# Kernel optimization log

Hardware: AMD Instinct MI355X
Metric: run time of the kernel (lower is better)

Reference implementation:

```python
import jax, jax.numpy as jnp
import numpy as np

D_IN = 256
DIMS = 256


def setup_inputs() -> dict:
    key = jax.random.key(0)
    k1, k2, k3, k4, k5 = jax.random.split(key, 5)
    B, Tq, Tk = 4, 512, 512
    query = jax.random.normal(k1, (B, Tq, D_IN), dtype=jnp.float32)
    value = jax.random.normal(k2, (B, Tk, D_IN), dtype=jnp.float32)
    # Dense(dims, use_bias=False) kernels (glorot-like scale) and AdditiveAttention scale vector
    Wq = jax.random.normal(k3, (D_IN, DIMS), dtype=jnp.float32) / np.sqrt(D_IN)
    Wv = jax.random.normal(k4, (D_IN, DIMS), dtype=jnp.float32) / np.sqrt(D_IN)
    scale = jax.random.normal(k5, (DIMS,), dtype=jnp.float32)
    return {"query": query, "value": value, "Wq": Wq, "Wv": Wv, "scale": scale}


def reference(query, value, Wq, Wv, scale):
    # q_proj: [B,Tq,d], k_proj: [B,Tk,d]; attention value = RAW value tensor (as in source)
    q = jnp.einsum("bqi,id->bqd", query, Wq)
    k = jnp.einsum("bki,id->bkd", value, Wv)
    # Additive (Bahdanau) scores: [B,Tq,Tk] via broadcast tanh then reduce with scale
    scores = jnp.einsum("bqkd,d->bqk", jnp.tanh(q[:, :, None, :] + k[:, None, :, :]), scale)
    attn = jax.nn.softmax(scores, axis=-1)  # masks are all-ones -> no-op
    out = jnp.einsum("bqk,bki->bqi", attn, value)
    return out, attn
```

## Files before the change

### kernel.cpp

```cpp
#include <hip/hip_runtime.h>

#define LOG2E 1.4426950408889634f
#define TWO_LOG2E 2.885390081777927f

__device__ __forceinline__ float fast_exp2(float x) { return __builtin_amdgcn_exp2f(x); }
__device__ __forceinline__ float fast_rcp(float x)  { return __builtin_amdgcn_rcpf(x); }

__device__ __forceinline__ void term2(float s0, float s1, float qx, float qy,
                                      float kx, float ky, float& acc) {
    const float A = fmaf(qx, kx, 1.f);
    const float B = fmaf(qy, ky, 1.f);
    acc = fmaf(fmaf(s1, A, s0 * B), fast_rcp(A * B), acc);
}

__global__ __launch_bounds__(256) void proj_kernel(
    const float* __restrict__ query, const float* __restrict__ value,
    const float* __restrict__ Wq, const float* __restrict__ Wv,
    float* __restrict__ eq, float* __restrict__ ekT)
{
    __shared__ float in_lds[8 * 256];
    const int t = threadIdx.x;
    const int row0 = blockIdx.x * 8;
    const float* src; const float* W;
    if (row0 < 2048) { src = query + (size_t)row0 * 256; W = Wq; }
    else { src = value + (size_t)(row0 - 2048) * 256; W = Wv; }

    const float4* s4 = (const float4*)src;
    float4* l4 = (float4*)in_lds;
    l4[t] = s4[t];
    l4[t + 256] = s4[t + 256];
    __syncthreads();

    float acc[8];
#pragma unroll
    for (int r = 0; r < 8; ++r) acc[r] = 0.f;

    for (int d = 0; d < 256; d += 4) {
        const float w0 = W[(d + 0) * 256 + t];
        const float w1 = W[(d + 1) * 256 + t];
        const float w2 = W[(d + 2) * 256 + t];
        const float w3 = W[(d + 3) * 256 + t];
#pragma unroll
        for (int r = 0; r < 8; ++r) {
            const float4 v = *(const float4*)&in_lds[r * 256 + d];
            acc[r] = fmaf(v.x, w0, acc[r]);
            acc[r] = fmaf(v.y, w1, acc[r]);
            acc[r] = fmaf(v.z, w2, acc[r]);
            acc[r] = fmaf(v.w, w3, acc[r]);
        }
    }

    if (row0 < 2048) {
        float* dst = eq + (size_t)row0 * 256;
#pragma unroll
        for (int r = 0; r < 8; ++r) dst[r * 256 + t] = fast_exp2(acc[r] * TWO_LOG2E);
    } else {
        const int r0 = row0 - 2048;
        const int bb = r0 >> 9, kin = r0 & 511;
        float* dstT = ekT + (size_t)bb * 131072 + (size_t)t * 512 + kin;
        float4 v0, v1;
        v0.x = fast_exp2(acc[0] * TWO_LOG2E); v0.y = fast_exp2(acc[1] * TWO_LOG2E);
        v0.z = fast_exp2(acc[2] * TWO_LOG2E); v0.w = fast_exp2(acc[3] * TWO_LOG2E);
        v1.x = fast_exp2(acc[4] * TWO_LOG2E); v1.y = fast_exp2(acc[5] * TWO_LOG2E);
        v1.z = fast_exp2(acc[6] * TWO_LOG2E); v1.w = fast_exp2(acc[7] * TWO_LOG2E);
        *(float4*)dstT = v0;
        *(float4*)(dstT + 4) = v1;
    }
}

#define EQ_ST 260
#define SS_ST 520
__global__ __launch_bounds__(512, 4) void fused_kernel(
    const float* __restrict__ eq, const float* __restrict__ ekT,
    const float* __restrict__ scale, const float* __restrict__ value,
    float* __restrict__ attn, float* __restrict__ out)
{
    __shared__ float eq_lds[4 * EQ_ST];
    __shared__ float sc_lds[256];
    __shared__ float s_tile[4 * SS_ST];
    __shared__ float red[4 * 4 * 256];
    __shared__ float inv_lds[4];

    const int t = threadIdx.x;
    const int w = t >> 6, lane = t & 63;
    const int qg = w >> 2;
    const int kg = ((w & 3) << 6) + lane;
    const int k0 = 2 * kg;
    const int qt = blockIdx.x, b = blockIdx.y;
    const int q0 = qt * 4;

    if (t < 256) {
        const int row = t >> 6, c = t & 63;
        const float4 v = ((const float4*)(eq + (size_t)(b * 512 + q0) * 256))[t];
        *(float4*)&eq_lds[row * EQ_ST + 4 * c] = v;
    } else {
        sc_lds[t - 256] = -2.f * scale[t - 256];
    }
    __syncthreads();

    const float* ekTb = ekT + (size_t)b * 131072;
    const float* q0r = &eq_lds[(2 * qg + 0) * EQ_ST];
    const float* q1r = &eq_lds[(2 * qg + 1) * EQ_ST];

    float a00 = 0.f, a01 = 0.f, a10 = 0.f, a11 = 0.f;

    float4 sv  = *(const float4*)&sc_lds[0];
    float4 qv0 = *(const float4*)&q0r[0];
    float4 qv1 = *(const float4*)&q1r[0];
    float2 k0v = *(const float2*)&ekTb[(size_t)0 * 512 + k0];
    float2 k1v = *(const float2*)&ekTb[(size_t)1 * 512 + k0];
    float2 k2v = *(const float2*)&ekTb[(size_t)2 * 512 + k0];
    float2 k3v = *(const float2*)&ekTb[(size_t)3 * 512 + k0];

#pragma unroll 4
    for (int d = 0; d < 256; d += 4) {
        const float4 csv = sv, c0 = qv0, c1 = qv1;
        const float2 ck0 = k0v, ck1 = k1v, ck2 = k2v, ck3 = k3v;

        if (d < 252) {
            const int dn = d + 4;
            sv  = *(const float4*)&sc_lds[dn];
            qv0 = *(const float4*)&q0r[dn];
            qv1 = *(const float4*)&q1r[dn];
            k0v = *(const float2*)&ekTb[(size_t)(dn + 0) * 512 + k0];
            k1v = *(const float2*)&ekTb[(size_t)(dn + 1) * 512 + k0];
            k2v = *(const float2*)&ekTb[(size_t)(dn + 2) * 512 + k0];
            k3v = *(const float2*)&ekTb[(size_t)(dn + 3) * 512 + k0];
        }

        term2(csv.x, csv.y, c0.x, c0.y, ck0.x, ck1.x, a00);
        term2(csv.z, csv.w, c0.z, c0.w, ck2.x, ck3.x, a00);
        term2(csv.x, csv.y, c0.x, c0.y, ck0.y, ck1.y, a01);
        term2(csv.z, csv.w, c0.z, c0.w, ck2.y, ck3.y, a01);

        term2(csv.x, csv.y, c1.x, c1.y, ck0.x, ck1.x, a10);
        term2(csv.z, csv.w, c1.z, c1.w, ck2.x, ck3.x, a10);
        term2(csv.x, csv.y, c1.x, c1.y, ck0.y, ck1.y, a11);
        term2(csv.z, csv.w, c1.z, c1.w, ck2.y, ck3.y, a11);
    }

    *(float2*)&s_tile[(2 * qg + 0) * SS_ST + k0] = make_float2(a00, a01);
    *(float2*)&s_tile[(2 * qg + 1) * SS_ST + k0] = make_float2(a10, a11);
    __syncthreads();

    if (w < 4) {
        float x[8];
        float m = -1e30f;
#pragma unroll
        for (int j = 0; j < 8; ++j) {
            x[j] = s_tile[w * SS_ST + 64 * j + lane];
            m = fmaxf(m, x[j]);
        }
#pragma unroll
        for (int off = 32; off; off >>= 1) m = fmaxf(m, __shfl_xor(m, off));

        float sum = 0.f;
#pragma unroll
        for (int j = 0; j < 8; ++j) { x[j] = fast_exp2((x[j] - m) * LOG2E); sum += x[j]; }
#pragma unroll
        for (int off = 32; off; off >>= 1) sum += __shfl_xor(sum, off);
        const float inv = fast_rcp(sum);

        float* arow = attn + (size_t)(b * 512 + q0 + w) * 512;
#pragma unroll
        for (int j = 0; j < 8; ++j) {
            s_tile[w * SS_ST + 64 * j + lane] = x[j];
            arow[64 * j + lane] = x[j] * inv;
        }
        if (lane == 0) inv_lds[w] = inv;
    }
    __syncthreads();

    float4 acc[4];
#pragma unroll
    for (int r = 0; r < 4; ++r) acc[r] = make_float4(0.f, 0.f, 0.f, 0.f);

    const float* vbase = value + (size_t)(b * 512 + 64 * w) * 256;
    for (int k4 = 0; k4 < 64; k4 += 4) {
        const float4 v0 = *(const float4*)&vbase[(k4 + 0) * 256 + lane * 4];
        const float4 v1 = *(const float4*)&vbase[(k4 + 1) * 256 + lane * 4];
        const float4 v2 = *(const float4*)&vbase[(k4 + 2) * 256 + lane * 4];
        const float4 v3 = *(const float4*)&vbase[(k4 + 3) * 256 + lane * 4];
#pragma unroll
        for (int r = 0; r < 4; ++r) {
            const float4 s4 = *(const float4*)&s_tile[r * SS_ST + 64 * w + k4];
            acc[r].x = fmaf(s4.x, v0.x, acc[r].x); acc[r].y = fmaf(s4.x, v0.y, acc[r].y);
            acc[r].z = fmaf(s4.x, v0.z, acc[r].z); acc[r].w = fmaf(s4.x, v0.w, acc[r].w);
            acc[r].x = fmaf(s4.y, v1.x, acc[r].x); acc[r].y = fmaf(s4.y, v1.y, acc[r].y);
            acc[r].z = fmaf(s4.y, v1.z, acc[r].z); acc[r].w = fmaf(s4.y, v1.w, acc[r].w);
            acc[r].x = fmaf(s4.z, v2.x, acc[r].x); acc[r].y = fmaf(s4.z, v2.y, acc[r].y);
            acc[r].z = fmaf(s4.z, v2.z, acc[r].z); acc[r].w = fmaf(s4.z, v2.w, acc[r].w);
            acc[r].x = fmaf(s4.w, v3.x, acc[r].x); acc[r].y = fmaf(s4.w, v3.y, acc[r].y);
            acc[r].z = fmaf(s4.w, v3.z, acc[r].z); acc[r].w = fmaf(s4.w, v3.w, acc[r].w);
        }
    }

    if (w >= 4) {
#pragma unroll
        for (int r = 0; r < 4; ++r)
            *(float4*)&red[((w - 4) * 4 + r) * 256 + lane * 4] = acc[r];
    }
    __syncthreads();
    if (w < 4) {
#pragma unroll
        for (int r = 0; r < 4; ++r) {
            const float4 o = *(const float4*)&red[(w * 4 + r) * 256 + lane * 4];
            acc[r].x += o.x; acc[r].y += o.y; acc[r].z += o.z; acc[r].w += o.w;
        }
    }
    __syncthreads();
    if (w >= 2 && w < 4) {
#pragma unroll
        for (int r = 0; r < 4; ++r)
            *(float4*)&red[((w - 2) * 4 + r) * 256 + lane * 4] = acc[r];
    }
    __syncthreads();
    if (w < 2) {
#pragma unroll
        for (int r = 0; r < 4; ++r) {
            const float4 o = *(const float4*)&red[(w * 4 + r) * 256 + lane * 4];
            acc[r].x += o.x; acc[r].y += o.y; acc[r].z += o.z; acc[r].w += o.w;
        }
    }
    __syncthreads();
    if (w == 1) {
#pragma unroll
        for (int r = 0; r < 4; ++r)
            *(float4*)&red[r * 256 + lane * 4] = acc[r];
    }
    __syncthreads();
    if (w == 0) {
#pragma unroll
        for (int r = 0; r < 4; ++r) {
            const float4 o = *(const float4*)&red[r * 256 + lane * 4];
            const float iv = inv_lds[r];
            float4 res;
            res.x = (acc[r].x + o.x) * iv;
            res.y = (acc[r].y + o.y) * iv;
            res.z = (acc[r].z + o.z) * iv;
            res.w = (acc[r].w + o.w) * iv;
            *(float4*)&out[(size_t)(b * 512 + q0 + r) * 256 + lane * 4] = res;
        }
    }
}

extern "C" void kernel_launch(void* const* d_in, const int* in_sizes, int n_in,
                              void* d_out, int out_size, void* d_ws, size_t ws_size,
                              hipStream_t stream) {
    const float* query = (const float*)d_in[0];
    const float* value = (const float*)d_in[1];
    const float* Wq    = (const float*)d_in[2];
    const float* Wv    = (const float*)d_in[3];
    const float* scale = (const float*)d_in[4];

    float* out0 = (float*)d_out;
    float* attn = out0 + 4 * 512 * 256;

    float* eq  = (float*)d_ws;
    float* ekT = eq + 2048 * 256;

    proj_kernel<<<512, 256, 0, stream>>>(query, value, Wq, Wv, eq, ekT);
    fused_kernel<<<dim3(128, 4), 512, 0, stream>>>(eq, ekT, scale, value, attn, out0);
}
```

Measured before the change: 74.25 us.

## Tile value projection with coalesced transposed stores and halve fused block size

The value-projection half of proj_kernel now uses a 64x32 LDS-tiled GEMM and stages its output through LDS, so the transposed ekT writes are coalesced float4 rows instead of strided per-thread writes. The fused kernel drops from 512 to 256 threads per block, with each thread computing all four query rows against its two keys. This reuses each ekT load across four queries rather than two and removes one level of the cross-wave output reduction. The cost is more registers per thread and fewer waves per block for hiding latency.

```diff
diff --git a/kernel.cpp b/kernel.cpp
--- a/kernel.cpp
+++ b/kernel.cpp
@@ -19,58 +19,110 @@
     float* __restrict__ eq, float* __restrict__ ekT)
 {
     __shared__ float in_lds[8 * 256];
+    __shared__ float v_lds[64 * 68];
+    __shared__ float w_lds[64 * 36];
+    __shared__ float t_lds[32 * 68];
+
     const int t = threadIdx.x;
-    const int row0 = blockIdx.x * 8;
-    const float* src; const float* W;
-    if (row0 < 2048) { src = query + (size_t)row0 * 256; W = Wq; }
-    else { src = value + (size_t)(row0 - 2048) * 256; W = Wv; }
-
-    const float4* s4 = (const float4*)src;
-    float4* l4 = (float4*)in_lds;
-    l4[t] = s4[t];
-    l4[t + 256] = s4[t + 256];
-    __syncthreads();
-
-    float acc[8];
-#pragma unroll
-    for (int r = 0; r < 8; ++r) acc[r] = 0.f;
-
-    for (int d = 0; d < 256; d += 4) {
-        const float w0 = W[(d + 0) * 256 + t];
-        const float w1 = W[(d + 1) * 256 + t];
-        const float w2 = W[(d + 2) * 256 + t];
-        const float w3 = W[(d + 3) * 256 + t];
-#pragma unroll
-        for (int r = 0; r < 8; ++r) {
-            const float4 v = *(const float4*)&in_lds[r * 256 + d];
-            acc[r] = fmaf(v.x, w0, acc[r]);
-            acc[r] = fmaf(v.y, w1, acc[r]);
-            acc[r] = fmaf(v.z, w2, acc[r]);
-            acc[r] = fmaf(v.w, w3, acc[r]);
-        }
-    }
-
-    if (row0 < 2048) {
+    const int bx = blockIdx.x;
+
+    if (bx < 256) {
+        const int row0 = bx * 8;
+        const float4* s4 = (const float4*)(query + (size_t)row0 * 256);
+        float4* l4 = (float4*)in_lds;
+        l4[t] = s4[t];
+        l4[t + 256] = s4[t + 256];
+        __syncthreads();
+
+        float acc[8];
+#pragma unroll
+        for (int r = 0; r < 8; ++r) acc[r] = 0.f;
+
+        for (int d = 0; d < 256; d += 4) {
+            const float w0 = Wq[(d + 0) * 256 + t];
+            const float w1 = Wq[(d + 1) * 256 + t];
+            const float w2 = Wq[(d + 2) * 256 + t];
+            const float w3 = Wq[(d + 3) * 256 + t];
+#pragma unroll
+            for (int r = 0; r < 8; ++r) {
+                const float4 v = *(const float4*)&in_lds[r * 256 + d];
+                acc[r] = fmaf(v.x, w0, acc[r]);
+                acc[r] = fmaf(v.y, w1, acc[r]);
+                acc[r] = fmaf(v.z, w2, acc[r]);
+                acc[r] = fmaf(v.w, w3, acc[r]);
+            }
+        }
         float* dst = eq + (size_t)row0 * 256;
 #pragma unroll
         for (int r = 0; r < 8; ++r) dst[r * 256 + t] = fast_exp2(acc[r] * TWO_LOG2E);
     } else {
-        const int r0 = row0 - 2048;
-        const int bb = r0 >> 9, kin = r0 & 511;
-        float* dstT = ekT + (size_t)bb * 131072 + (size_t)t * 512 + kin;
-        float4 v0, v1;
-        v0.x = fast_exp2(acc[0] * TWO_LOG2E); v0.y = fast_exp2(acc[1] * TWO_LOG2E);
-        v0.z = fast_exp2(acc[2] * TWO_LOG2E); v0.w = fast_exp2(acc[3] * TWO_LOG2E);
-        v1.x = fast_exp2(acc[4] * TWO_LOG2E); v1.y = fast_exp2(acc[5] * TWO_LOG2E);
-        v1.z = fast_exp2(acc[6] * TWO_LOG2E); v1.w = fast_exp2(acc[7] * TWO_LOG2E);
-        *(float4*)dstT = v0;
-        *(float4*)(dstT + 4) = v1;
+        const int bi = bx - 256;
+        const int kt = bi >> 3, dt = bi & 7;
+        const int gk0 = kt * 64;
+        const int bb = gk0 >> 9, kin0 = gk0 & 511;
+        const int dout0 = dt * 32;
+        const int kp = t >> 3, dg = t & 7;
+
+        float acc[2][4];
+#pragma unroll
+        for (int i = 0; i < 2; ++i)
+#pragma unroll
+            for (int j = 0; j < 4; ++j) acc[i][j] = 0.f;
+
+        for (int dc = 0; dc < 256; dc += 64) {
+            __syncthreads();
+#pragma unroll
+            for (int l = 0; l < 4; ++l) {
+                const int idx = t + 256 * l;
+                const int r = idx >> 4, c4 = (idx & 15) * 4;
+                *(float4*)&v_lds[r * 68 + c4] =
+                    *(const float4*)&value[(size_t)(gk0 + r) * 256 + dc + c4];
+            }
+#pragma unroll
+            for (int l = 0; l < 2; ++l) {
+                const int idx = t + 256 * l;
+                const int r = idx >> 3, c4 = (idx & 7) * 4;
+                *(float4*)&w_lds[r * 36 + c4] =
+                    *(const float4*)&Wv[(size_t)(dc + r) * 256 + dout0 + c4];
+            }
+            __syncthreads();
+
+#pragma unroll 8
+            for (int din = 0; din < 64; ++din) {
+                const float v0 = v_lds[(2 * kp + 0) * 68 + din];
+                const float v1 = v_lds[(2 * kp + 1) * 68 + din];
+                const float4 wv = *(const float4*)&w_lds[din * 36 + 4 * dg];
+                acc[0][0] = fmaf(v0, wv.x, acc[0][0]);
+                acc[0][1] = fmaf(v0, wv.y, acc[0][1]);
+                acc[0][2] = fmaf(v0, wv.z, acc[0][2]);
+                acc[0][3] = fmaf(v0, wv.w, acc[0][3]);
+                acc[1][0] = fmaf(v1, wv.x, acc[1][0]);
+                acc[1][1] = fmaf(v1, wv.y, acc[1][1]);
+                acc[1][2] = fmaf(v1, wv.z, acc[1][2]);
+                acc[1][3] = fmaf(v1, wv.w, acc[1][3]);
+            }
+        }
+        __syncthreads();
+#pragma unroll
+        for (int i = 0; i < 2; ++i)
+#pragma unroll
+            for (int j = 0; j < 4; ++j)
+                t_lds[(4 * dg + j) * 68 + 2 * kp + i] =
+                    fast_exp2(acc[i][j] * TWO_LOG2E);
+        __syncthreads();
+#pragma unroll
+        for (int l = 0; l < 2; ++l) {
+            const int idx = t + 256 * l;
+            const int row = idx >> 4, c4 = (idx & 15) * 4;
+            *(float4*)&ekT[(size_t)bb * 131072 + (size_t)(dout0 + row) * 512 + kin0 + c4] =
+                *(const float4*)&t_lds[row * 68 + c4];
+        }
     }
 }
 
 #define EQ_ST 260
 #define SS_ST 520
-__global__ __launch_bounds__(512, 4) void fused_kernel(
+__global__ __launch_bounds__(256, 3) void fused_kernel(
     const float* __restrict__ eq, const float* __restrict__ ekT,
     const float* __restrict__ scale, const float* __restrict__ value,
     float* __restrict__ attn, float* __restrict__ out)
@@ -78,43 +130,46 @@
     __shared__ float eq_lds[4 * EQ_ST];
     __shared__ float sc_lds[256];
     __shared__ float s_tile[4 * SS_ST];
-    __shared__ float red[4 * 4 * 256];
+    __shared__ float red[2 * 4 * 256];
     __shared__ float inv_lds[4];
 
     const int t = threadIdx.x;
     const int w = t >> 6, lane = t & 63;
-    const int qg = w >> 2;
-    const int kg = ((w & 3) << 6) + lane;
+    const int kg = (w << 6) + lane;
     const int k0 = 2 * kg;
     const int qt = blockIdx.x, b = blockIdx.y;
     const int q0 = qt * 4;
 
-    if (t < 256) {
+    {
+        const float4 v = ((const float4*)(eq + (size_t)(b * 512 + q0) * 256))[t];
         const int row = t >> 6, c = t & 63;
-        const float4 v = ((const float4*)(eq + (size_t)(b * 512 + q0) * 256))[t];
         *(float4*)&eq_lds[row * EQ_ST + 4 * c] = v;
-    } else {
-        sc_lds[t - 256] = -2.f * scale[t - 256];
-    }
-    __syncthreads();
-
-    const float* ekTb = ekT + (size_t)b * 131072;
-    const float* q0r = &eq_lds[(2 * qg + 0) * EQ_ST];
-    const float* q1r = &eq_lds[(2 * qg + 1) * EQ_ST];
+    }
+    sc_lds[t] = -2.f * scale[t];
+    __syncthreads();
+
+    const float* ekTb = ekT + (size_t)b * 131072 + k0;
+    const float* q0r = &eq_lds[0 * EQ_ST];
+    const float* q1r = &eq_lds[1 * EQ_ST];
+    const float* q2r = &eq_lds[2 * EQ_ST];
+    const float* q3r = &eq_lds[3 * EQ_ST];
 
     float a00 = 0.f, a01 = 0.f, a10 = 0.f, a11 = 0.f;
+    float a20 = 0.f, a21 = 0.f, a30 = 0.f, a31 = 0.f;
 
     float4 sv  = *(const float4*)&sc_lds[0];
     float4 qv0 = *(const float4*)&q0r[0];
     float4 qv1 = *(const float4*)&q1r[0];
-    float2 k0v = *(const float2*)&ekTb[(size_t)0 * 512 + k0];
-    float2 k1v = *(const float2*)&ekTb[(size_t)1 * 512 + k0];
-    float2 k2v = *(const float2*)&ekTb[(size_t)2 * 512 + k0];
-    float2 k3v = *(const float2*)&ekTb[(size_t)3 * 512 + k0];
+    float4 qv2 = *(const float4*)&q2r[0];
+    float4 qv3 = *(const float4*)&q3r[0];
+    float2 k0v = *(const float2*)&ekTb[(size_t)0 * 512];
+    float2 k1v = *(const float2*)&ekTb[(size_t)1 * 512];
+    float2 k2v = *(const float2*)&ekTb[(size_t)2 * 512];
+    float2 k3v = *(const float2*)&ekTb[(size_t)3 * 512];
 
 #pragma unroll 4
     for (int d = 0; d < 256; d += 4) {
-        const float4 csv = sv, c0 = qv0, c1 = qv1;
+        const float4 csv = sv, c0 = qv0, c1 = qv1, c2 = qv2, c3 = qv3;
         const float2 ck0 = k0v, ck1 = k1v, ck2 = k2v, ck3 = k3v;
 
         if (d < 252) {
@@ -122,10 +177,12 @@
             sv  = *(const float4*)&sc_lds[dn];
             qv0 = *(const float4*)&q0r[dn];
             qv1 = *(const float4*)&q1r[dn];
-            k0v = *(const float2*)&ekTb[(size_t)(dn + 0) * 512 + k0];
-            k1v = *(const float2*)&ekTb[(size_t)(dn + 1) * 512 + k0];
-            k2v = *(const float2*)&ekTb[(size_t)(dn + 2) * 512 + k0];
-            k3v = *(const float2*)&ekTb[(size_t)(dn + 3) * 512 + k0];
+            qv2 = *(const float4*)&q2r[dn];
+            qv3 = *(const float4*)&q3r[dn];
+            k0v = *(const float2*)&ekTb[(size_t)(dn + 0) * 512];
+            k1v = *(const float2*)&ekTb[(size_t)(dn + 1) * 512];
+            k2v = *(const float2*)&ekTb[(size_t)(dn + 2) * 512];
+            k3v = *(const float2*)&ekTb[(size_t)(dn + 3) * 512];
         }
 
         term2(csv.x, csv.y, c0.x, c0.y, ck0.x, ck1.x, a00);
@@ -137,13 +194,25 @@
         term2(csv.z, csv.w, c1.z, c1.w, ck2.x, ck3.x, a10);
         term2(csv.x, csv.y, c1.x, c1.y, ck0.y, ck1.y, a11);
         term2(csv.z, csv.w, c1.z, c1.w, ck2.y, ck3.y, a11);
-    }
-
-    *(float2*)&s_tile[(2 * qg + 0) * SS_ST + k0] = make_float2(a00, a01);
-    *(float2*)&s_tile[(2 * qg + 1) * SS_ST + k0] = make_float2(a10, a11);
-    __syncthreads();
-
-    if (w < 4) {
+
+        term2(csv.x, csv.y, c2.x, c2.y, ck0.x, ck1.x, a20);
+        term2(csv.z, csv.w, c2.z, c2.w, ck2.x, ck3.x, a20);
+        term2(csv.x, csv.y, c2.x, c2.y, ck0.y, ck1.y, a21);
+        term2(csv.z, csv.w, c2.z, c2.w, ck2.y, ck3.y, a21);
+
+        term2(csv.x, csv.y, c3.x, c3.y, ck0.x, ck1.x, a30);
+        term2(csv.z, csv.w, c3.z, c3.w, ck2.x, ck3.x, a30);
+        term2(csv.x, csv.y, c3.x, c3.y, ck0.y, ck1.y, a31);
+        term2(csv.z, csv.w, c3.z, c3.w, ck2.y, ck3.y, a31);
+    }
+
+    *(float2*)&s_tile[0 * SS_ST + k0] = make_float2(a00, a01);
+    *(float2*)&s_tile[1 * SS_ST + k0] = make_float2(a10, a11);
+    *(float2*)&s_tile[2 * SS_ST + k0] = make_float2(a20, a21);
+    *(float2*)&s_tile[3 * SS_ST + k0] = make_float2(a30, a31);
+    __syncthreads();
+
+    {
         float x[8];
         float m = -1e30f;
 #pragma unroll
@@ -175,15 +244,15 @@
 #pragma unroll
     for (int r = 0; r < 4; ++r) acc[r] = make_float4(0.f, 0.f, 0.f, 0.f);
 
-    const float* vbase = value + (size_t)(b * 512 + 64 * w) * 256;
-    for (int k4 = 0; k4 < 64; k4 += 4) {
+    const float* vbase = value + (size_t)(b * 512 + 128 * w) * 256;
+    for (int k4 = 0; k4 < 128; k4 += 4) {
         const float4 v0 = *(const float4*)&vbase[(k4 + 0) * 256 + lane * 4];
         const float4 v1 = *(const float4*)&vbase[(k4 + 1) * 256 + lane * 4];
         const float4 v2 = *(const float4*)&vbase[(k4 + 2) * 256 + lane * 4];
         const float4 v3 = *(const float4*)&vbase[(k4 + 3) * 256 + lane * 4];
 #pragma unroll
         for (int r = 0; r < 4; ++r) {
-            const float4 s4 = *(const float4*)&s_tile[r * SS_ST + 64 * w + k4];
+            const float4 s4 = *(const float4*)&s_tile[r * SS_ST + 128 * w + k4];
             acc[r].x = fmaf(s4.x, v0.x, acc[r].x); acc[r].y = fmaf(s4.x, v0.y, acc[r].y);
             acc[r].z = fmaf(s4.x, v0.z, acc[r].z); acc[r].w = fmaf(s4.x, v0.w, acc[r].w);
             acc[r].x = fmaf(s4.y, v1.x, acc[r].x); acc[r].y = fmaf(s4.y, v1.y, acc[r].y);
@@ -195,21 +264,7 @@
         }
     }
 
-    if (w >= 4) {
-#pragma unroll
-        for (int r = 0; r < 4; ++r)
-            *(float4*)&red[((w - 4) * 4 + r) * 256 + lane * 4] = acc[r];
-    }
-    __syncthreads();
-    if (w < 4) {
-#pragma unroll
-        for (int r = 0; r < 4; ++r) {
-            const float4 o = *(const float4*)&red[(w * 4 + r) * 256 + lane * 4];
-            acc[r].x += o.x; acc[r].y += o.y; acc[r].z += o.z; acc[r].w += o.w;
-        }
-    }
-    __syncthreads();
-    if (w >= 2 && w < 4) {
+    if (w >= 2) {
 #pragma unroll
         for (int r = 0; r < 4; ++r)
             *(float4*)&red[((w - 2) * 4 + r) * 256 + lane * 4] = acc[r];
@@ -260,5 +315,5 @@
     float* ekT = eq + 2048 * 256;
 
     proj_kernel<<<512, 256, 0, stream>>>(query, value, Wq, Wv, eq, ekT);
-    fused_kernel<<<dim3(128, 4), 512, 0, stream>>>(eq, ekT, scale, value, attn, out0);
+    fused_kernel<<<dim3(128, 4), 256, 0, stream>>>(eq, ekT, scale, value, attn, out0);
 }
```

Result: faster. 65.10 us (-12.3%).
